# Optimization experiments

Measured on AMD Instinct MI355X. Metric: run time of the kernel, lower is better.

The kernel has to match this reference:

```python
import jax, jax.numpy as jnp
import numpy as np

N_NODES = 50000
N_EDGES = 600000
D = 128
HEADS = 4
CH = D // HEADS  # 32 channels per head
NEG_SLOPE = 0.2


def setup_inputs() -> dict:
    key = jax.random.key(0)
    ks = jax.random.split(key, 16)
    x = jax.random.normal(ks[0], (N_NODES, D), dtype=jnp.float32)
    # edges with src != dst so that appending self-loops matches PyG's
    # remove_self_loops + add_self_loops exactly
    src = jax.random.randint(ks[1], (N_EDGES,), 0, N_NODES, dtype=jnp.int32)
    off = jax.random.randint(ks[2], (N_EDGES,), 1, N_NODES, dtype=jnp.int32)
    dst = (src + off) % N_NODES
    edge_index = jnp.stack([src, dst], axis=0)
    s = 1.0 / np.sqrt(D)
    def layer_params(k):
        k1, k2, k3, k4 = jax.random.split(k, 4)
        return (jax.random.normal(k1, (D, D), jnp.float32) * s,
                jax.random.normal(k2, (HEADS, CH), jnp.float32) * s,
                jax.random.normal(k3, (HEADS, CH), jnp.float32) * s,
                jnp.zeros((D,), jnp.float32),
                jax.random.normal(k4, (D, D), jnp.float32) * s)
    W1, att_src1, att_dst1, bias1, Wskip1 = layer_params(ks[3])
    W2, att_src2, att_dst2, bias2, Wskip2 = layer_params(ks[4])
    return dict(x=x, edge_index=edge_index,
                W1=W1, att_src1=att_src1, att_dst1=att_dst1, bias1=bias1, Wskip1=Wskip1,
                W2=W2, att_src2=att_src2, att_dst2=att_dst2, bias2=bias2, Wskip2=Wskip2)


def _gat_block(x, src, dst, W, a_src, a_dst, bias, Wskip):
    N = x.shape[0]
    h = (x @ W).reshape(N, HEADS, CH)                       # [N,H,C]
    asrc = jnp.einsum('nhc,hc->nh', h, a_src)               # [N,H]
    adst = jnp.einsum('nhc,hc->nh', h, a_dst)
    e = jax.nn.leaky_relu(asrc[src] + adst[dst], NEG_SLOPE)  # [E,H]
    m = jax.ops.segment_max(e, dst, num_segments=N)
    m = jnp.where(jnp.isfinite(m), m, 0.0)                  # guard empty segments
    e = jnp.exp(e - m[dst])
    denom = jax.ops.segment_sum(e, dst, num_segments=N)
    alpha = e / (denom[dst] + 1e-16)                        # segment softmax over dst
    msg = h[src] * alpha[:, :, None]                        # [E,H,C]
    agg = jax.ops.segment_sum(msg, dst, num_segments=N)
    out = agg.reshape(N, D) + bias + x @ Wskip              # conv + skip
    return jax.nn.elu(out)


def reference(x, edge_index, W1, att_src1, att_dst1, bias1, Wskip1,
              W2, att_src2, att_dst2, bias2, Wskip2):
    N = x.shape[0]
    loops = jnp.arange(N, dtype=edge_index.dtype)
    src = jnp.concatenate([edge_index[0], loops])
    dst = jnp.concatenate([edge_index[1], loops])
    x = _gat_block(x, src, dst, W1, att_src1, att_dst1, bias1, Wskip1)
    x = _gat_block(x, src, dst, W2, att_src2, att_dst2, bias2, Wskip2)
    return x
```

## Files before the change

kernel.cpp:

```cpp
#include <hip/hip_runtime.h>
#include <hip/hip_bf16.h>

#define NN 50000
#define NE 600000
#define DD 128
#define NH 4
#define ET (NE + NN)
#define NEG_SLOPE 0.2f
#define NB 196

typedef __attribute__((ext_vector_type(8))) short short8;
typedef __attribute__((ext_vector_type(4))) float f32x4;

__device__ __forceinline__ float bf2f(unsigned short u) {
    union { unsigned int i; float f; } c; c.i = ((unsigned int)u) << 16; return c.f;
}
__device__ __forceinline__ unsigned short f2bf(float f) {
    union { float f; unsigned int i; } c; c.f = f;
    unsigned int r = c.i + 0x7FFF + ((c.i >> 16) & 1);
    return (unsigned short)(r >> 16);
}


__global__ void __launch_bounds__(256) prep_k(const float* __restrict__ W1, const float* __restrict__ Ws1,
                                              const float* __restrict__ W2, const float* __restrict__ Ws2,
                                              unsigned short* __restrict__ Wt, int* __restrict__ counts) {
    int idx = blockIdx.x * 256 + threadIdx.x;
    int mat = idx >> 14;
    int p = idx & 16383;
    int col = p >> 7;
    int cs = (p >> 3) & 15;
    int j = p & 7;
    int c = cs ^ (col & 7);
    int k = c * 8 + j;
    const float* Wsrc = (mat == 0) ? W1 : (mat == 1) ? Ws1 : (mat == 2) ? W2 : Ws2;
    Wt[idx] = f2bf(Wsrc[k * DD + col]);
    if (idx < NN) counts[idx] = 0;
}


__global__ void __launch_bounds__(256) partial_k(const int* __restrict__ counts, int* __restrict__ bsum) {
    __shared__ int tmp[256];
    int t = blockIdx.x * 256 + threadIdx.x;
    int v = (t < NN) ? counts[t] + 1 : 0;
    tmp[threadIdx.x] = v;
    __syncthreads();
    for (int off = 128; off > 0; off >>= 1) {
        if (threadIdx.x < off) tmp[threadIdx.x] += tmp[threadIdx.x + off];
        __syncthreads();
    }
    if (threadIdx.x == 0) bsum[blockIdx.x] = tmp[0];
}

__global__ void __launch_bounds__(256) offsets_k(const int* __restrict__ counts, const int* __restrict__ bsum,
                                                 int* __restrict__ offsets, int* __restrict__ cursor,
                                                 int* __restrict__ esrc) {
    __shared__ int bs[256];
    __shared__ int tmp[256];
    int b = blockIdx.x, tid = threadIdx.x;
    int bv = (tid < NB) ? bsum[tid] : 0;
    bs[tid] = bv;
    __syncthreads();
    for (int off = 1; off < 256; off <<= 1) {
        int u = (tid >= off) ? bs[tid - off] : 0;
        __syncthreads();
        bs[tid] += u;
        __syncthreads();
    }
    int boff = (b == 0) ? 0 : bs[b - 1];

    int t = b * 256 + tid;
    int c = (t < NN) ? counts[t] : 0;
    int v = (t < NN) ? c + 1 : 0;
    tmp[tid] = v;
    __syncthreads();
    for (int off = 1; off < 256; off <<= 1) {
        int u = (tid >= off) ? tmp[tid - off] : 0;
        __syncthreads();
        tmp[tid] += u;
        __syncthreads();
    }
    if (t < NN) {
        int o = boff + tmp[tid] - v;
        offsets[t] = o;
        cursor[t] = o;
        esrc[o + c] = t;
    }
    if (b == 0 && tid == 0) offsets[NN] = ET;
}

__global__ void __launch_bounds__(256) scatter_k(const int* __restrict__ src, const int* __restrict__ dst,
                                                 int* __restrict__ cursor, int* __restrict__ esrc) {
    int e = blockIdx.x * 256 + threadIdx.x;
    if (e < NE) {
        int pos = atomicAdd(&cursor[dst[e]], 1);
        esrc[pos] = src[e];
    }
}


#define GGEMM ((NN + 127) / 128)

template <bool F32IN>
__global__ void __launch_bounds__(512) gemm2_k(const void* __restrict__ xin,
                                               const unsigned short* __restrict__ Wl,
                                               const float* __restrict__ a_src, const float* __restrict__ a_dst,
                                               unsigned short* __restrict__ h2, unsigned short* __restrict__ skipb,
                                               float* __restrict__ nsrc, float* __restrict__ ndst,
                                               const int* __restrict__ e_dst, int* __restrict__ counts) {
    __shared__ __align__(16) unsigned char wlds[65536];
    if (F32IN && blockIdx.x >= GGEMM) {
        int e = (blockIdx.x - GGEMM) * 512 + threadIdx.x;
        if (e < NE) atomicAdd(&counts[e_dst[e]], 1);
        return;
    }
    int row0 = blockIdx.x * 128;
    int tid = threadIdx.x;
    int w = tid >> 6, lidx = tid & 63;
    int lrow = lidx & 15, lk = lidx >> 4;
    int srow = row0 + w * 16 + lrow;
    int rclamp = srow < NN ? srow : NN - 1;

    short8 afrag[4];
    if (F32IN) {
        const float* xp = (const float*)xin + (size_t)rclamp * DD;
#pragma unroll
        for (int kc = 0; kc < 4; ++kc) {
            float4 u0 = *(const float4*)(xp + kc * 32 + lk * 8);
            float4 u1 = *(const float4*)(xp + kc * 32 + lk * 8 + 4);
            short8 a;
            a[0] = (short)f2bf(u0.x); a[1] = (short)f2bf(u0.y);
            a[2] = (short)f2bf(u0.z); a[3] = (short)f2bf(u0.w);
            a[4] = (short)f2bf(u1.x); a[5] = (short)f2bf(u1.y);
            a[6] = (short)f2bf(u1.z); a[7] = (short)f2bf(u1.w);
            afrag[kc] = a;
        }
    } else {
        const unsigned short* xp = (const unsigned short*)xin + (size_t)rclamp * DD;
#pragma unroll
        for (int kc = 0; kc < 4; ++kc)
            afrag[kc] = *(const short8*)(xp + kc * 32 + lk * 8);
    }

    {
        const uint4* g = (const uint4*)Wl;
        uint4* l = (uint4*)wlds;
#pragma unroll
        for (int i = 0; i < 8; ++i)
            l[i * 512 + tid] = g[i * 512 + tid];
    }
    __syncthreads();

    f32x4 zero = {0.f, 0.f, 0.f, 0.f};
    f32x4 acch[8], accs[8];
#pragma unroll
    for (int t = 0; t < 8; ++t) { acch[t] = zero; accs[t] = zero; }

#pragma unroll
    for (int kc = 0; kc < 4; ++kc) {
        short8 a = afrag[kc];
#pragma unroll
        for (int t = 0; t < 8; ++t) {
            int off = (t * 16 + lrow) * 256 + (((kc * 4 + lk) ^ (lrow & 7)) * 16);
            short8 b  = *(const short8*)&wlds[off];
            short8 bs = *(const short8*)&wlds[off + 32768];
            acch[t] = __builtin_amdgcn_mfma_f32_16x16x32_bf16(a, b, acch[t], 0, 0, 0);
            accs[t] = __builtin_amdgcn_mfma_f32_16x16x32_bf16(a, bs, accs[t], 0, 0, 0);
        }
    }

#pragma unroll
    for (int t = 0; t < 8; ++t) {
#pragma unroll
        for (int q = 0; q < 4; ++q) {
            int grow = row0 + w * 16 + lk * 4 + q;
            if (grow < NN) {
                int col = t * 16 + lrow;
                h2[(size_t)grow * DD + col] = f2bf(acch[t][q]);
                skipb[(size_t)grow * DD + col] = f2bf(accs[t][q]);
            }
        }
    }

    float as_lo[NH], as_hi[NH], ad_lo[NH], ad_hi[NH];
#pragma unroll
    for (int h = 0; h < NH; ++h) {
        as_lo[h] = a_src[h * 32 + lrow];
        as_hi[h] = a_src[h * 32 + 16 + lrow];
        ad_lo[h] = a_dst[h * 32 + lrow];
        ad_hi[h] = a_dst[h * 32 + 16 + lrow];
    }
#pragma unroll
    for (int h = 0; h < NH; ++h) {
#pragma unroll
        for (int q = 0; q < 4; ++q) {
            float ps = acch[2 * h][q] * as_lo[h] + acch[2 * h + 1][q] * as_hi[h];
            float pd = acch[2 * h][q] * ad_lo[h] + acch[2 * h + 1][q] * ad_hi[h];
#pragma unroll
            for (int off = 1; off < 16; off <<= 1) {
                ps += __shfl_xor(ps, off);
                pd += __shfl_xor(pd, off);
            }
            if (lrow == 0) {
                int grow = row0 + w * 16 + lk * 4 + q;
                if (grow < NN) {
                    nsrc[grow * 4 + h] = ps;
                    ndst[grow * 4 + h] = pd;
                }
            }
        }
    }
}


__global__ void __launch_bounds__(256) aggregate_k(const unsigned short* __restrict__ h2,
                                                   const unsigned short* __restrict__ skipb,
                                                   const float* __restrict__ nsrc, const float* __restrict__ ndst,
                                                   const int* __restrict__ offsets, const int* __restrict__ esrc,
                                                   const float* __restrict__ bias, float* __restrict__ outf,
                                                   unsigned short* __restrict__ outb) {
    int n = blockIdx.x * 4 + (threadIdx.x >> 6);
    int i = threadIdx.x & 63;
    int e = i & 15, hc = i >> 4;
    int gbase = i & 48;
    int beg = offsets[n], end = offsets[n + 1];
    float ad = ndst[n * 4 + hc];
    const unsigned int* h2w = (const unsigned int*)h2;

    float m = -1e30f, den = 0.f, acc0 = 0.f, acc1 = 0.f;
    for (int base = beg; base < end; base += 16) {
        int j = base + e;
        int jc = j < end ? j : end - 1;
        int s = esrc[jc];
        float a = nsrc[s * 4 + hc] + ad;
        a = a > 0.f ? a : NEG_SLOPE * a;
        if (j >= end) a = -1e30f;
        float cm = a;
        cm = fmaxf(cm, __shfl_xor(cm, 1));
        cm = fmaxf(cm, __shfl_xor(cm, 2));
        cm = fmaxf(cm, __shfl_xor(cm, 4));
        cm = fmaxf(cm, __shfl_xor(cm, 8));
        float mn = fmaxf(m, cm);
        float scale = __expf(m - mn);
        float wgt = __expf(a - mn);
        m = mn;
        float sw = wgt;
        sw += __shfl_xor(sw, 1);
        sw += __shfl_xor(sw, 2);
        sw += __shfl_xor(sw, 4);
        sw += __shfl_xor(sw, 8);
        den = den * scale + sw;
        acc0 *= scale;
        acc1 *= scale;
#pragma unroll
        for (int e2 = 0; e2 < 16; ++e2) {
            int se = __shfl(s, e2);
            float we = __shfl(wgt, gbase + e2);
            unsigned hv = h2w[se * 64 + i];
            acc0 = fmaf(we, bf2f((unsigned short)(hv & 0xFFFF)), acc0);
            acc1 = fmaf(we, bf2f((unsigned short)(hv >> 16)), acc1);
        }
    }
    float inv = 1.f / (den + 1e-16f);
    int c0 = 2 * i;
    unsigned sk = ((const unsigned int*)skipb)[n * 64 + i];
    float2 bv = *(const float2*)&bias[c0];
    float o0 = acc0 * inv + bv.x + bf2f((unsigned short)(sk & 0xFFFF));
    float o1 = acc1 * inv + bv.y + bf2f((unsigned short)(sk >> 16));
    o0 = o0 > 0.f ? o0 : expm1f(o0);
    o1 = o1 > 0.f ? o1 : expm1f(o1);
    size_t o = (size_t)n * DD;
    if (outf) { outf[o + c0] = o0; outf[o + c0 + 1] = o1; }
    if (outb) { outb[o + c0] = f2bf(o0); outb[o + c0 + 1] = f2bf(o1); }
}


extern "C" void kernel_launch(void* const* d_in, const int* in_sizes, int n_in,
                              void* d_out, int out_size, void* d_ws, size_t ws_size,
                              hipStream_t stream) {
    const float* x   = (const float*)d_in[0];
    const int* eidx  = (const int*)d_in[1];
    const float* W1  = (const float*)d_in[2];
    const float* as1 = (const float*)d_in[3];
    const float* ad1 = (const float*)d_in[4];
    const float* b1  = (const float*)d_in[5];
    const float* Ws1 = (const float*)d_in[6];
    const float* W2  = (const float*)d_in[7];
    const float* as2 = (const float*)d_in[8];
    const float* ad2 = (const float*)d_in[9];
    const float* b2  = (const float*)d_in[10];
    const float* Ws2 = (const float*)d_in[11];
    float* out = (float*)d_out;

    const int* e_src = eidx;
    const int* e_dst = eidx + NE;

    char* p = (char*)d_ws;
    unsigned short* h2    = (unsigned short*)p; p += (size_t)NN * DD * 2;
    unsigned short* xb    = (unsigned short*)p; p += (size_t)NN * DD * 2;
    unsigned short* skipb = (unsigned short*)p; p += (size_t)NN * DD * 2;
    float* nsrc = (float*)p; p += (size_t)NN * NH * 4;
    float* ndst = (float*)p; p += (size_t)NN * NH * 4;
    unsigned short* Wt = (unsigned short*)p; p += (size_t)4 * DD * DD * 2;
    int* counts  = (int*)p; p += (size_t)NN * 4;
    int* offsets = (int*)p; p += (size_t)(NN + 4) * 4;
    int* cursor  = (int*)p; p += (size_t)NN * 4;
    int* bsum    = (int*)p; p += 256 * 4;
    int* esrc    = (int*)p; p += (size_t)ET * 4;

    const int CB = (NE + 511) / 512;

    prep_k<<<256, 256, 0, stream>>>(W1, Ws1, W2, Ws2, Wt, counts);

    gemm2_k<true><<<GGEMM + CB, 512, 0, stream>>>(x, Wt, as1, ad1, h2, skipb, nsrc, ndst, e_dst, counts);

    partial_k<<<NB, 256, 0, stream>>>(counts, bsum);
    offsets_k<<<NB, 256, 0, stream>>>(counts, bsum, offsets, cursor, esrc);
    scatter_k<<<(NE + 255) / 256, 256, 0, stream>>>(e_src, e_dst, cursor, esrc);

    aggregate_k<<<NN / 4, 256, 0, stream>>>(h2, skipb, nsrc, ndst, offsets, esrc, b1, nullptr, xb);

    gemm2_k<false><<<GGEMM, 512, 0, stream>>>(xb, Wt + 32768, as2, ad2, h2, skipb, nsrc, ndst, e_dst, counts);
    aggregate_k<<<NN / 4, 256, 0, stream>>>(h2, skipb, nsrc, ndst, offsets, esrc, b2, out, nullptr);
}
```

Before: 250.0 us.

## Batch gather loads in aggregate and fold degree counting into GEMM blocks

The aggregate kernel's inner loop is split into three phases: shuffle all 16 source indices and weights, issue up to 16 independent h2 gathers, then accumulate. This raises memory-level parallelism, and tail slots are skipped. Per-node attention scalars are now read as a float4 and the head is picked in registers. The degree-count atomics move from separate extra blocks into a strided loop at the start of every GEMM block, which shrinks the grid but serialises the counting work ahead of each block's GEMM. The batched loads use more registers, which may lower occupancy.

```diff
diff --git a/kernel.cpp b/kernel.cpp
--- a/kernel.cpp
+++ b/kernel.cpp
@@ -19,6 +19,9 @@
     union { float f; unsigned int i; } c; c.f = f;
     unsigned int r = c.i + 0x7FFF + ((c.i >> 16) & 1);
     return (unsigned short)(r >> 16);
+}
+__device__ __forceinline__ float sel4(float4 v, int hc) {
+    return (hc & 2) ? ((hc & 1) ? v.w : v.z) : ((hc & 1) ? v.y : v.x);
 }
 
 
@@ -109,13 +112,17 @@
                                                float* __restrict__ nsrc, float* __restrict__ ndst,
                                                const int* __restrict__ e_dst, int* __restrict__ counts) {
     __shared__ __align__(16) unsigned char wlds[65536];
-    if (F32IN && blockIdx.x >= GGEMM) {
-        int e = (blockIdx.x - GGEMM) * 512 + threadIdx.x;
-        if (e < NE) atomicAdd(&counts[e_dst[e]], 1);
-        return;
-    }
+    int tid = threadIdx.x;
+
+    if (F32IN) {
+        const int EPB = (NE + GGEMM - 1) / GGEMM;
+        int e0 = blockIdx.x * EPB;
+        int e1 = e0 + EPB < NE ? e0 + EPB : NE;
+        for (int ee = e0 + tid; ee < e1; ee += 512)
+            atomicAdd(&counts[e_dst[ee]], 1);
+    }
+
     int row0 = blockIdx.x * 128;
-    int tid = threadIdx.x;
     int w = tid >> 6, lidx = tid & 63;
     int lrow = lidx & 15, lk = lidx >> 4;
     int srow = row0 + w * 16 + lrow;
@@ -224,7 +231,8 @@
     int e = i & 15, hc = i >> 4;
     int gbase = i & 48;
     int beg = offsets[n], end = offsets[n + 1];
-    float ad = ndst[n * 4 + hc];
+    float4 ndv = *(const float4*)&ndst[n * 4];
+    float ad = sel4(ndv, hc);
     const unsigned int* h2w = (const unsigned int*)h2;
 
     float m = -1e30f, den = 0.f, acc0 = 0.f, acc1 = 0.f;
@@ -232,7 +240,8 @@
         int j = base + e;
         int jc = j < end ? j : end - 1;
         int s = esrc[jc];
-        float a = nsrc[s * 4 + hc] + ad;
+        float4 nv = *(const float4*)&nsrc[s * 4];
+        float a = sel4(nv, hc) + ad;
         a = a > 0.f ? a : NEG_SLOPE * a;
         if (j >= end) a = -1e30f;
         float cm = a;
@@ -252,14 +261,23 @@
         den = den * scale + sw;
         acc0 *= scale;
         acc1 *= scale;
+
+        int cnt = end - base; cnt = cnt < 16 ? cnt : 16;
+        int sse[16]; float wwe[16]; unsigned hv[16];
 #pragma unroll
         for (int e2 = 0; e2 < 16; ++e2) {
-            int se = __shfl(s, e2);
-            float we = __shfl(wgt, gbase + e2);
-            unsigned hv = h2w[se * 64 + i];
-            acc0 = fmaf(we, bf2f((unsigned short)(hv & 0xFFFF)), acc0);
-            acc1 = fmaf(we, bf2f((unsigned short)(hv >> 16)), acc1);
-        }
+            sse[e2] = __shfl(s, e2);
+            wwe[e2] = __shfl(wgt, gbase + e2);
+        }
+#pragma unroll
+        for (int e2 = 0; e2 < 16; ++e2)
+            if (e2 < cnt) hv[e2] = h2w[sse[e2] * 64 + i];
+#pragma unroll
+        for (int e2 = 0; e2 < 16; ++e2)
+            if (e2 < cnt) {
+                acc0 = fmaf(wwe[e2], bf2f((unsigned short)(hv[e2] & 0xFFFF)), acc0);
+                acc1 = fmaf(wwe[e2], bf2f((unsigned short)(hv[e2] >> 16)), acc1);
+            }
     }
     float inv = 1.f / (den + 1e-16f);
     int c0 = 2 * i;
@@ -308,11 +326,9 @@
     int* bsum    = (int*)p; p += 256 * 4;
     int* esrc    = (int*)p; p += (size_t)ET * 4;
 
-    const int CB = (NE + 511) / 512;
-
     prep_k<<<256, 256, 0, stream>>>(W1, Ws1, W2, Ws2, Wt, counts);
 
-    gemm2_k<true><<<GGEMM + CB, 512, 0, stream>>>(x, Wt, as1, ad1, h2, skipb, nsrc, ndst, e_dst, counts);
+    gemm2_k<true><<<GGEMM, 512, 0, stream>>>(x, Wt, as1, ad1, h2, skipb, nsrc, ndst, e_dst, counts);
 
     partial_k<<<NB, 256, 0, stream>>>(counts, bsum);
     offsets_k<<<NB, 256, 0, stream>>>(counts, bsum, offsets, cursor, esrc);
```

Result: slower. 297.4 us (+18.9%).
